# Performance work log

Hardware: AMD Instinct MI355X
Metric: run time of the kernel (lower is better)

The kernel has to match this reference:

```python
import jax, jax.numpy as jnp
import numpy as np

R = 5  # box filter radius (self.r)
EPS = 0.01


def box_filter(x, r):
    # depthwise (groups=C) box filter, kernel (2r+1)x(2r+1), zero padding r
    c = x.shape[1]
    k = 2 * r + 1
    w = jnp.full((c, 1, k, k), 1.0 / (k * k), dtype=x.dtype)
    return jax.lax.conv_general_dilated(
        x, w, window_strides=(1, 1), padding=[(r, r), (r, r)],
        dimension_numbers=("NCHW", "OIHW", "NCHW"), feature_group_count=c)


def setup_inputs() -> dict:
    key = jax.random.key(0)
    x = jax.random.normal(key, (4, 64, 256, 256), dtype=jnp.float32)
    return {"x": x}


def reference(x):
    _, _, H, W = x.shape
    # normalization map accounting for zero-padded borders
    N = box_filter(jnp.ones((1, 1, H, W), dtype=x.dtype), R)  # [1,1,H,W]
    mean_x = box_filter(x, R) / N
    var_x = box_filter(x * x, R) / N - mean_x * mean_x
    A = var_x / (var_x + EPS)
    b = (1.0 - A) * mean_x
    m = A * x + b
    return x * m
```

## Files before the change

### kernel.cpp

```cpp
#include <hip/hip_runtime.h>
#include <hip/hip_bf16.h>


#define RAD    5
#define KW     11
#define IMG_H  256
#define IMG_W  256
#define TILE_H 8
#define IN_H   (TILE_H + 2 * RAD)
#define STRIPS (IMG_H / TILE_H)
#define EPS_F  0.01f

__global__ __launch_bounds__(256)
void AdaGuidedFilter_17686675325295_kernel(const float* __restrict__ x,
                                           float* __restrict__ out) {
    __shared__ float2 vsum[TILE_H * IMG_W];

    const int d     = blockIdx.x;
    const int L     = (d & 7) * ((256 * STRIPS) / 8) + (d >> 3);
    const int img   = L >> 5;
    const int strip = L & (STRIPS - 1);
    const int tid   = threadIdx.x;

    const float* __restrict__ xim = x   + (size_t)img * (IMG_H * IMG_W);
    float* __restrict__       oim = out + (size_t)img * (IMG_H * IMG_W);

    const int row0 = strip * TILE_H - RAD;

    {
        float xr[IN_H];
        if (strip != 0 && strip != STRIPS - 1) {
            #pragma unroll
            for (int li = 0; li < IN_H; ++li)
                xr[li] = xim[(size_t)(row0 + li) * IMG_W + tid];
        } else {
            #pragma unroll
            for (int li = 0; li < IN_H; ++li) {
                const int g = row0 + li;
                xr[li] = (g >= 0 && g < IMG_H) ? xim[(size_t)g * IMG_W + tid] : 0.0f;
            }
        }

        float s = 0.0f, s2 = 0.0f;
        #pragma unroll
        for (int li = 0; li < KW; ++li) { s += xr[li]; s2 = fmaf(xr[li], xr[li], s2); }

        #pragma unroll
        for (int r = 0; r < TILE_H; ++r) {
            vsum[(r << 8) | (tid ^ r)] = make_float2(s, s2);
            if (r < TILE_H - 1) {
                const float a = xr[r + KW], b0 = xr[r];
                s  += a - b0;
                s2 += a * a - b0 * b0;
            }
        }
    }
    __syncthreads();

    const int lr  = tid & 7;
    const int seg = tid >> 3;
    const int c0  = seg * 8;
    const int gr  = strip * TILE_H + lr;

    float xv[8];
    {
        const float4* p = reinterpret_cast<const float4*>(xim + (size_t)gr * IMG_W + c0);
        const float4 q0 = p[0], q1 = p[1];
        xv[0]=q0.x; xv[1]=q0.y; xv[2]=q0.z; xv[3]=q0.w;
        xv[4]=q1.x; xv[5]=q1.y; xv[6]=q1.z; xv[7]=q1.w;
    }

    const int rlo = (gr - RAD < 0) ? 0 : gr - RAD;
    const int rhi = (gr + RAD > IMG_H - 1) ? IMG_H - 1 : gr + RAD;
    const float rcnt = (float)(rhi - rlo + 1);

    float o[8];
    if (seg >= 1 && seg <= 30) {
        float s = 0.0f, s2 = 0.0f;
        #pragma unroll
        for (int dd = -RAD; dd <= RAD; ++dd) {
            const float2 v = vsum[(lr << 8) | ((c0 + dd) ^ lr)];
            s += v.x; s2 += v.y;
        }
        const float inv = __builtin_amdgcn_rcpf(rcnt * 11.0f);
        #pragma unroll
        for (int i = 0; i < 8; ++i) {
            const float mean = s * inv;
            const float m2   = s2 * inv;
            const float var  = fmaf(-mean, mean, m2);
            const float A    = var * __builtin_amdgcn_rcpf(var + EPS_F);
            const float xq   = xv[i];
            o[i] = xq * fmaf(A, xq - mean, mean);
            if (i < 7) {
                const float2 va = vsum[(lr << 8) | ((c0 + i + RAD + 1) ^ lr)];
                const float2 vb = vsum[(lr << 8) | ((c0 + i - RAD) ^ lr)];
                s  += va.x - vb.x;
                s2 += va.y - vb.y;
            }
        }
    } else {
        float s = 0.0f, s2 = 0.0f;
        #pragma unroll
        for (int dd = -RAD; dd <= RAD; ++dd) {
            const int cc = c0 + dd;
            if (cc >= 0 && cc < IMG_W) {
                const float2 v = vsum[(lr << 8) | (cc ^ lr)];
                s += v.x; s2 += v.y;
            }
        }
        #pragma unroll
        for (int i = 0; i < 8; ++i) {
            const int c   = c0 + i;
            const int wlo = (c - RAD < 0) ? 0 : c - RAD;
            const int whi = (c + RAD > IMG_W - 1) ? IMG_W - 1 : c + RAD;
            const float inv  = __builtin_amdgcn_rcpf(rcnt * (float)(whi - wlo + 1));
            const float mean = s * inv;
            const float m2   = s2 * inv;
            const float var  = fmaf(-mean, mean, m2);
            const float A    = var * __builtin_amdgcn_rcpf(var + EPS_F);
            const float xq   = xv[i];
            o[i] = xq * fmaf(A, xq - mean, mean);
            if (i < 7) {
                const int ca = c + RAD + 1;
                const int cs = c - RAD;
                if (ca < IMG_W) { const float2 v = vsum[(lr << 8) | (ca ^ lr)]; s += v.x; s2 += v.y; }
                if (cs >= 0)    { const float2 v = vsum[(lr << 8) | (cs ^ lr)]; s -= v.x; s2 -= v.y; }
            }
        }
    }

    float4* orow = reinterpret_cast<float4*>(oim + (size_t)gr * IMG_W + c0);
    orow[0] = make_float4(o[0], o[1], o[2], o[3]);
    orow[1] = make_float4(o[4], o[5], o[6], o[7]);
}

extern "C" void kernel_launch(void* const* d_in, const int* in_sizes, int n_in,
                              void* d_out, int out_size, void* d_ws, size_t ws_size,
                              hipStream_t stream) {
    (void)in_sizes; (void)n_in; (void)d_ws; (void)ws_size; (void)out_size;
    const float* x = (const float*)d_in[0];
    float* out = (float*)d_out;
    dim3 grid(256 * STRIPS);
    dim3 block(256);
    AdaGuidedFilter_17686675325295_kernel<<<grid, block, 0, stream>>>(x, out);
}
```

Baseline: 29.13 us.

## Process taller strips per block with rolling vertical sums in chunks

Each block now covers a 32-row strip instead of 8 rows. It keeps a register ring buffer of 11 rows so the vertical running sum slides down the strip, and handles it in four 8-row chunks that reuse one shared-memory buffer. This cuts the redundant halo-row reads from 10 extra rows per 8 output rows to 10 per 32. In exchange the grid has four times fewer blocks, each chunk adds barriers, and the horizontal pass waits on the vertical pass inside each block.

```diff
diff --git a/kernel.cpp b/kernel.cpp
--- a/kernel.cpp
+++ b/kernel.cpp
@@ -6,70 +6,21 @@
 #define KW     11
 #define IMG_H  256
 #define IMG_W  256
-#define TILE_H 8
-#define IN_H   (TILE_H + 2 * RAD)
+#define TILE_H 32
+#define CHUNK  8
+#define NCHUNK (TILE_H / CHUNK)
 #define STRIPS (IMG_H / TILE_H)
+#define NBLK   (256 * STRIPS)
 #define EPS_F  0.01f
 
-__global__ __launch_bounds__(256)
-void AdaGuidedFilter_17686675325295_kernel(const float* __restrict__ x,
-                                           float* __restrict__ out) {
-    __shared__ float2 vsum[TILE_H * IMG_W];
+__device__ __forceinline__ float ldrow(const float* __restrict__ xim, int g, int c) {
+    return (g >= 0 && g < IMG_H) ? xim[(size_t)g * IMG_W + c] : 0.0f;
+}
 
-    const int d     = blockIdx.x;
-    const int L     = (d & 7) * ((256 * STRIPS) / 8) + (d >> 3);
-    const int img   = L >> 5;
-    const int strip = L & (STRIPS - 1);
-    const int tid   = threadIdx.x;
-
-    const float* __restrict__ xim = x   + (size_t)img * (IMG_H * IMG_W);
-    float* __restrict__       oim = out + (size_t)img * (IMG_H * IMG_W);
-
-    const int row0 = strip * TILE_H - RAD;
-
-    {
-        float xr[IN_H];
-        if (strip != 0 && strip != STRIPS - 1) {
-            #pragma unroll
-            for (int li = 0; li < IN_H; ++li)
-                xr[li] = xim[(size_t)(row0 + li) * IMG_W + tid];
-        } else {
-            #pragma unroll
-            for (int li = 0; li < IN_H; ++li) {
-                const int g = row0 + li;
-                xr[li] = (g >= 0 && g < IMG_H) ? xim[(size_t)g * IMG_W + tid] : 0.0f;
-            }
-        }
-
-        float s = 0.0f, s2 = 0.0f;
-        #pragma unroll
-        for (int li = 0; li < KW; ++li) { s += xr[li]; s2 = fmaf(xr[li], xr[li], s2); }
-
-        #pragma unroll
-        for (int r = 0; r < TILE_H; ++r) {
-            vsum[(r << 8) | (tid ^ r)] = make_float2(s, s2);
-            if (r < TILE_H - 1) {
-                const float a = xr[r + KW], b0 = xr[r];
-                s  += a - b0;
-                s2 += a * a - b0 * b0;
-            }
-        }
-    }
-    __syncthreads();
-
-    const int lr  = tid & 7;
-    const int seg = tid >> 3;
-    const int c0  = seg * 8;
-    const int gr  = strip * TILE_H + lr;
-
-    float xv[8];
-    {
-        const float4* p = reinterpret_cast<const float4*>(xim + (size_t)gr * IMG_W + c0);
-        const float4 q0 = p[0], q1 = p[1];
-        xv[0]=q0.x; xv[1]=q0.y; xv[2]=q0.z; xv[3]=q0.w;
-        xv[4]=q1.x; xv[5]=q1.y; xv[6]=q1.z; xv[7]=q1.w;
-    }
-
+__device__ __forceinline__ void half_pass(const float2* __restrict__ vsum,
+                                          float* __restrict__ oim,
+                                          const float* xv,
+                                          int lr, int seg, int c0, int gr) {
     const int rlo = (gr - RAD < 0) ? 0 : gr - RAD;
     const int rhi = (gr + RAD > IMG_H - 1) ? IMG_H - 1 : gr + RAD;
     const float rcnt = (float)(rhi - rlo + 1);
@@ -134,13 +85,84 @@
     orow[1] = make_float4(o[4], o[5], o[6], o[7]);
 }
 
+template<bool CHECKED>
+__device__ __forceinline__ void run_strip(const float* __restrict__ xim,
+                                          float* __restrict__ oim,
+                                          float2* __restrict__ vsum,
+                                          int strip, int tid) {
+    const int row0 = strip * TILE_H - RAD;
+    const int lr   = tid & 7;
+    const int seg  = tid >> 3;
+    const int c0   = seg * 8;
+
+    float ring[KW];
+    #pragma unroll
+    for (int i = 0; i < KW; ++i)
+        ring[i] = CHECKED ? ldrow(xim, row0 + i, tid)
+                          : xim[(size_t)(row0 + i) * IMG_W + tid];
+
+    float s = 0.0f, s2 = 0.0f;
+    #pragma unroll
+    for (int i = 0; i < KW; ++i) { s += ring[i]; s2 = fmaf(ring[i], ring[i], s2); }
+
+    #pragma unroll
+    for (int k = 0; k < NCHUNK; ++k) {
+        #pragma unroll
+        for (int rr = 0; rr < CHUNK; ++rr) {
+            const int r = k * CHUNK + rr;
+            vsum[(rr << 8) | (tid ^ rr)] = make_float2(s, s2);
+            if (r < TILE_H - 1) {
+                const float old = ring[r % KW];
+                const float a   = CHECKED ? ldrow(xim, row0 + KW + r, tid)
+                                          : xim[(size_t)(row0 + KW + r) * IMG_W + tid];
+                s  += a - old;
+                s2  = fmaf(a, a, fmaf(-old, old, s2));
+                ring[r % KW] = a;
+            }
+        }
+
+        const int gr = strip * TILE_H + k * CHUNK + lr;
+        float xv[8];
+        {
+            const float4* p = reinterpret_cast<const float4*>(xim + (size_t)gr * IMG_W + c0);
+            const float4 q0 = p[0], q1 = p[1];
+            xv[0]=q0.x; xv[1]=q0.y; xv[2]=q0.z; xv[3]=q0.w;
+            xv[4]=q1.x; xv[5]=q1.y; xv[6]=q1.z; xv[7]=q1.w;
+        }
+
+        __syncthreads();
+        half_pass(vsum, oim, xv, lr, seg, c0, gr);
+        if (k < NCHUNK - 1) __syncthreads();
+    }
+}
+
+__global__ __launch_bounds__(256)
+void AdaGuidedFilter_17686675325295_kernel(const float* __restrict__ x,
+                                           float* __restrict__ out) {
+    __shared__ float2 vsum[CHUNK * IMG_W];
+
+    const int d     = blockIdx.x;
+    const int L     = (d & 7) * (NBLK / 8) + (d >> 3);
+    const int img   = L >> 3;
+    const int strip = L & (STRIPS - 1);
+    const int tid   = threadIdx.x;
+
+    const float* __restrict__ xim = x   + (size_t)img * (IMG_H * IMG_W);
+    float* __restrict__       oim = out + (size_t)img * (IMG_H * IMG_W);
+
+    if (strip != 0 && strip != STRIPS - 1)
+        run_strip<false>(xim, oim, vsum, strip, tid);
+    else
+        run_strip<true>(xim, oim, vsum, strip, tid);
+}
+
 extern "C" void kernel_launch(void* const* d_in, const int* in_sizes, int n_in,
                               void* d_out, int out_size, void* d_ws, size_t ws_size,
                               hipStream_t stream) {
     (void)in_sizes; (void)n_in; (void)d_ws; (void)ws_size; (void)out_size;
     const float* x = (const float*)d_in[0];
     float* out = (float*)d_out;
-    dim3 grid(256 * STRIPS);
+    dim3 grid(NBLK);
     dim3 block(256);
     AdaGuidedFilter_17686675325295_kernel<<<grid, block, 0, stream>>>(x, out);
 }
```

Result: slower. 35.88 us (+23.2%).

## Split vertical pass across half the threads with float2 loads and packed math

Applied to the files above, without the earlier changes.

The vertical box-sum pass now runs on only the first 128 threads. Each handles two adjacent columns using 8-byte vector loads and packed f32x2 arithmetic, and writes float4 entries into the swizzled shared buffer. The other 128 threads issue their own row loads for the horizontal stage at the same time, so global loads from both stages overlap. The interior horizontal pass is restructured to compute two output columns per step with packed two-wide ops, aiming at v_pk_fma/v_pk_mul use. The cost is an imbalanced first phase where half the threads sit idle until the barrier.

```diff
diff --git a/kernel.cpp b/kernel.cpp
--- a/kernel.cpp
+++ b/kernel.cpp
@@ -9,7 +9,10 @@
 #define TILE_H 8
 #define IN_H   (TILE_H + 2 * RAD)
 #define STRIPS (IMG_H / TILE_H)
+#define NBLK   (256 * STRIPS)
 #define EPS_F  0.01f
+
+typedef float f32x2 __attribute__((ext_vector_type(2)));
 
 __global__ __launch_bounds__(256)
 void AdaGuidedFilter_17686675325295_kernel(const float* __restrict__ x,
@@ -17,58 +20,75 @@
     __shared__ float2 vsum[TILE_H * IMG_W];
 
     const int d     = blockIdx.x;
-    const int L     = (d & 7) * ((256 * STRIPS) / 8) + (d >> 3);
+    const int L     = (d & 7) * (NBLK / 8) + (d >> 3);
     const int img   = L >> 5;
     const int strip = L & (STRIPS - 1);
-    const int tid   = threadIdx.x;
+    const int t     = threadIdx.x;
 
     const float* __restrict__ xim = x   + (size_t)img * (IMG_H * IMG_W);
     float* __restrict__       oim = out + (size_t)img * (IMG_H * IMG_W);
 
     const int row0 = strip * TILE_H - RAD;
+    const bool rowcheck = (strip == 0) || (strip == STRIPS - 1);
 
-    {
-        float xr[IN_H];
-        if (strip != 0 && strip != STRIPS - 1) {
-            #pragma unroll
-            for (int li = 0; li < IN_H; ++li)
-                xr[li] = xim[(size_t)(row0 + li) * IMG_W + tid];
-        } else {
-            #pragma unroll
-            for (int li = 0; li < IN_H; ++li) {
-                const int g = row0 + li;
-                xr[li] = (g >= 0 && g < IMG_H) ? xim[(size_t)g * IMG_W + tid] : 0.0f;
-            }
-        }
-
-        float s = 0.0f, s2 = 0.0f;
-        #pragma unroll
-        for (int li = 0; li < KW; ++li) { s += xr[li]; s2 = fmaf(xr[li], xr[li], s2); }
-
-        #pragma unroll
-        for (int r = 0; r < TILE_H; ++r) {
-            vsum[(r << 8) | (tid ^ r)] = make_float2(s, s2);
-            if (r < TILE_H - 1) {
-                const float a = xr[r + KW], b0 = xr[r];
-                s  += a - b0;
-                s2 += a * a - b0 * b0;
-            }
-        }
-    }
-    __syncthreads();
-
-    const int lr  = tid & 7;
-    const int seg = tid >> 3;
+    const int lr  = t & 7;
+    const int seg = t >> 3;
     const int c0  = seg * 8;
     const int gr  = strip * TILE_H + lr;
 
     float xv[8];
-    {
+    if (t >= 128) {
         const float4* p = reinterpret_cast<const float4*>(xim + (size_t)gr * IMG_W + c0);
         const float4 q0 = p[0], q1 = p[1];
         xv[0]=q0.x; xv[1]=q0.y; xv[2]=q0.z; xv[3]=q0.w;
         xv[4]=q1.x; xv[5]=q1.y; xv[6]=q1.z; xv[7]=q1.w;
     }
+
+    if (t < 128) {
+        const int cc0 = t << 1;
+        f32x2 xr[IN_H];
+        if (!rowcheck) {
+            #pragma unroll
+            for (int li = 0; li < IN_H; ++li)
+                xr[li] = *reinterpret_cast<const f32x2*>(xim + (size_t)(row0 + li) * IMG_W + cc0);
+        } else {
+            #pragma unroll
+            for (int li = 0; li < IN_H; ++li) {
+                const int g = row0 + li;
+                if (g >= 0 && g < IMG_H)
+                    xr[li] = *reinterpret_cast<const f32x2*>(xim + (size_t)g * IMG_W + cc0);
+                else
+                    xr[li] = (f32x2){0.0f, 0.0f};
+            }
+        }
+
+        f32x2 s = {0.0f, 0.0f}, s2 = {0.0f, 0.0f};
+        #pragma unroll
+        for (int li = 0; li < KW; ++li) {
+            s += xr[li];
+            s2 = __builtin_elementwise_fma(xr[li], xr[li], s2);
+        }
+
+        float4* vs4 = reinterpret_cast<float4*>(vsum);
+        #pragma unroll
+        for (int r = 0; r < TILE_H; ++r) {
+            const int bi = (r << 7) | ((cc0 ^ r) >> 1);
+            if ((r & 1) == 0) vs4[bi] = make_float4(s.x, s2.x, s.y, s2.y);
+            else              vs4[bi] = make_float4(s.y, s2.y, s.x, s2.x);
+            if (r < TILE_H - 1) {
+                const f32x2 a = xr[r + KW], b = xr[r];
+                s  += a - b;
+                s2  = __builtin_elementwise_fma(a, a,
+                        __builtin_elementwise_fma(-b, b, s2));
+            }
+        }
+
+        const float4* p = reinterpret_cast<const float4*>(xim + (size_t)gr * IMG_W + c0);
+        const float4 q0 = p[0], q1 = p[1];
+        xv[0]=q0.x; xv[1]=q0.y; xv[2]=q0.z; xv[3]=q0.w;
+        xv[4]=q1.x; xv[5]=q1.y; xv[6]=q1.z; xv[7]=q1.w;
+    }
+    __syncthreads();
 
     const int rlo = (gr - RAD < 0) ? 0 : gr - RAD;
     const int rhi = (gr + RAD > IMG_H - 1) ? IMG_H - 1 : gr + RAD;
@@ -83,19 +103,35 @@
             s += v.x; s2 += v.y;
         }
         const float inv = __builtin_amdgcn_rcpf(rcnt * 11.0f);
+        const f32x2 inv2  = {inv, inv};
+        const f32x2 eps2  = {EPS_F, EPS_F};
+
         #pragma unroll
-        for (int i = 0; i < 8; ++i) {
-            const float mean = s * inv;
-            const float m2   = s2 * inv;
-            const float var  = fmaf(-mean, mean, m2);
-            const float A    = var * __builtin_amdgcn_rcpf(var + EPS_F);
-            const float xq   = xv[i];
-            o[i] = xq * fmaf(A, xq - mean, mean);
-            if (i < 7) {
-                const float2 va = vsum[(lr << 8) | ((c0 + i + RAD + 1) ^ lr)];
-                const float2 vb = vsum[(lr << 8) | ((c0 + i - RAD) ^ lr)];
-                s  += va.x - vb.x;
-                s2 += va.y - vb.y;
+        for (int g = 0; g < 4; ++g) {
+            const int ce = c0 + 2 * g;
+            const float2 va = vsum[(lr << 8) | ((ce + RAD + 1) ^ lr)];
+            const float2 vb = vsum[(lr << 8) | ((ce - RAD) ^ lr)];
+            const float so  = s  + va.x - vb.x;
+            const float s2o = s2 + va.y - vb.y;
+            const f32x2 SS   = {s, so};
+            const f32x2 SS2  = {s2, s2o};
+            const f32x2 mean = SS * inv2;
+            const f32x2 m2   = SS2 * inv2;
+            const f32x2 var  = __builtin_elementwise_fma(-mean, mean, m2);
+            const f32x2 den  = var + eps2;
+            const f32x2 rr   = {__builtin_amdgcn_rcpf(den.x), __builtin_amdgcn_rcpf(den.y)};
+            const f32x2 A    = var * rr;
+            const f32x2 xq   = {xv[2*g], xv[2*g+1]};
+            const f32x2 xm   = xq - mean;
+            const f32x2 tt   = __builtin_elementwise_fma(A, xm, mean);
+            const f32x2 oo   = xq * tt;
+            o[2*g]   = oo.x;
+            o[2*g+1] = oo.y;
+            if (g < 3) {
+                const float2 va2 = vsum[(lr << 8) | ((ce + RAD + 2) ^ lr)];
+                const float2 vb2 = vsum[(lr << 8) | ((ce - RAD + 1) ^ lr)];
+                s  = so  + va2.x - vb2.x;
+                s2 = s2o + va2.y - vb2.y;
             }
         }
     } else {
@@ -140,7 +176,7 @@
     (void)in_sizes; (void)n_in; (void)d_ws; (void)ws_size; (void)out_size;
     const float* x = (const float*)d_in[0];
     float* out = (float*)d_out;
-    dim3 grid(256 * STRIPS);
+    dim3 grid(NBLK);
     dim3 block(256);
     AdaGuidedFilter_17686675325295_kernel<<<grid, block, 0, stream>>>(x, out);
 }
```

After: 31.34 us. +7.6%, slower.

## Split tile into per-wavefront column slabs with halo to drop block barrier

Applied to the files above, without the earlier changes.

Each 64-lane wavefront now owns a 64-column slab and computes its own vertical sums, including a 10-column halo, into a private LDS region. The block-wide __syncthreads is replaced by an lgkmcnt wait, which relies on wavefront-synchronous execution. The aim is to remove block-level barrier stalls so wavefronts run independently. In exchange, halo columns are reloaded and summed redundantly (about 16% extra column work), and 10 lanes do a second column pass, which causes divergence.

```diff
diff --git a/kernel.cpp b/kernel.cpp
--- a/kernel.cpp
+++ b/kernel.cpp
@@ -9,79 +9,85 @@
 #define TILE_H 8
 #define IN_H   (TILE_H + 2 * RAD)
 #define STRIPS (IMG_H / TILE_H)
+#define NBLK   (256 * STRIPS)
+#define WSTR   80
 #define EPS_F  0.01f
 
-__global__ __launch_bounds__(256)
-void AdaGuidedFilter_17686675325295_kernel(const float* __restrict__ x,
-                                           float* __restrict__ out) {
-    __shared__ float2 vsum[TILE_H * IMG_W];
+__device__ __forceinline__ int swz(int co, int r) {
+    return (co & ~7) | ((co & 7) ^ r);
+}
 
-    const int d     = blockIdx.x;
-    const int L     = (d & 7) * ((256 * STRIPS) / 8) + (d >> 3);
-    const int img   = L >> 5;
-    const int strip = L & (STRIPS - 1);
-    const int tid   = threadIdx.x;
+template<bool ROWCHECK>
+__device__ __forceinline__ void colpass(const float* __restrict__ xim,
+                                        float2* __restrict__ vb,
+                                        int row0, int gc, bool colok, int co) {
+    float xr[IN_H];
+    #pragma unroll
+    for (int li = 0; li < IN_H; ++li) {
+        const int g = row0 + li;
+        const bool ok = colok && (!ROWCHECK || ((unsigned)g < (unsigned)IMG_H));
+        xr[li] = ok ? xim[(size_t)g * IMG_W + gc] : 0.0f;
+    }
+    float s = 0.0f, s2 = 0.0f;
+    #pragma unroll
+    for (int li = 0; li < KW; ++li) { s += xr[li]; s2 = fmaf(xr[li], xr[li], s2); }
+    #pragma unroll
+    for (int r = 0; r < TILE_H; ++r) {
+        vb[r * WSTR + swz(co, r)] = make_float2(s, s2);
+        if (r < TILE_H - 1) {
+            const float a = xr[r + KW], b = xr[r];
+            s  += a - b;
+            s2  = fmaf(a, a, fmaf(-b, b, s2));
+        }
+    }
+}
 
-    const float* __restrict__ xim = x   + (size_t)img * (IMG_H * IMG_W);
-    float* __restrict__       oim = out + (size_t)img * (IMG_H * IMG_W);
-
+template<bool ROWCHECK>
+__device__ __forceinline__ void run_tile(const float* __restrict__ xim,
+                                         float* __restrict__ oim,
+                                         float2* __restrict__ vb,
+                                         int strip, int C0, int l) {
     const int row0 = strip * TILE_H - RAD;
 
+    if (l < 10) {
+        const int gc = C0 + 59 + l;
+        colpass<ROWCHECK>(xim, vb, row0, gc, gc < IMG_W, 64 + l);
+    }
     {
-        float xr[IN_H];
-        if (strip != 0 && strip != STRIPS - 1) {
-            #pragma unroll
-            for (int li = 0; li < IN_H; ++li)
-                xr[li] = xim[(size_t)(row0 + li) * IMG_W + tid];
-        } else {
-            #pragma unroll
-            for (int li = 0; li < IN_H; ++li) {
-                const int g = row0 + li;
-                xr[li] = (g >= 0 && g < IMG_H) ? xim[(size_t)g * IMG_W + tid] : 0.0f;
-            }
-        }
+        const int gc = C0 - 5 + l;
+        colpass<ROWCHECK>(xim, vb, row0, gc, (unsigned)gc < (unsigned)IMG_W, l);
+    }
 
-        float s = 0.0f, s2 = 0.0f;
-        #pragma unroll
-        for (int li = 0; li < KW; ++li) { s += xr[li]; s2 = fmaf(xr[li], xr[li], s2); }
-
-        #pragma unroll
-        for (int r = 0; r < TILE_H; ++r) {
-            vsum[(r << 8) | (tid ^ r)] = make_float2(s, s2);
-            if (r < TILE_H - 1) {
-                const float a = xr[r + KW], b0 = xr[r];
-                s  += a - b0;
-                s2 += a * a - b0 * b0;
-            }
-        }
-    }
-    __syncthreads();
-
-    const int lr  = tid & 7;
-    const int seg = tid >> 3;
-    const int c0  = seg * 8;
-    const int gr  = strip * TILE_H + lr;
+    const int lr    = l & 7;
+    const int seg   = l >> 3;
+    const int gcol0 = C0 + seg * 8;
+    const int gr    = strip * TILE_H + lr;
 
     float xv[8];
     {
-        const float4* p = reinterpret_cast<const float4*>(xim + (size_t)gr * IMG_W + c0);
+        const float4* p = reinterpret_cast<const float4*>(xim + (size_t)gr * IMG_W + gcol0);
         const float4 q0 = p[0], q1 = p[1];
         xv[0]=q0.x; xv[1]=q0.y; xv[2]=q0.z; xv[3]=q0.w;
         xv[4]=q1.x; xv[5]=q1.y; xv[6]=q1.z; xv[7]=q1.w;
     }
 
+    asm volatile("s_waitcnt lgkmcnt(0)" ::: "memory");
+
     const int rlo = (gr - RAD < 0) ? 0 : gr - RAD;
     const int rhi = (gr + RAD > IMG_H - 1) ? IMG_H - 1 : gr + RAD;
     const float rcnt = (float)(rhi - rlo + 1);
 
+    const int cob = seg * 8;
+    float s = 0.0f, s2 = 0.0f;
+    #pragma unroll
+    for (int dd = 0; dd < KW; ++dd) {
+        const float2 v = vb[lr * WSTR + swz(cob + dd, lr)];
+        s += v.x; s2 += v.y;
+    }
+
     float o[8];
-    if (seg >= 1 && seg <= 30) {
-        float s = 0.0f, s2 = 0.0f;
-        #pragma unroll
-        for (int dd = -RAD; dd <= RAD; ++dd) {
-            const float2 v = vsum[(lr << 8) | ((c0 + dd) ^ lr)];
-            s += v.x; s2 += v.y;
-        }
+    const bool edge = (C0 == 0 && seg == 0) || (C0 == 192 && seg == 7);
+    if (!edge) {
         const float inv = __builtin_amdgcn_rcpf(rcnt * 11.0f);
         #pragma unroll
         for (int i = 0; i < 8; ++i) {
@@ -92,25 +98,16 @@
             const float xq   = xv[i];
             o[i] = xq * fmaf(A, xq - mean, mean);
             if (i < 7) {
-                const float2 va = vsum[(lr << 8) | ((c0 + i + RAD + 1) ^ lr)];
-                const float2 vb = vsum[(lr << 8) | ((c0 + i - RAD) ^ lr)];
-                s  += va.x - vb.x;
-                s2 += va.y - vb.y;
+                const float2 va = vb[lr * WSTR + swz(cob + i + KW, lr)];
+                const float2 vs = vb[lr * WSTR + swz(cob + i, lr)];
+                s  += va.x - vs.x;
+                s2 += va.y - vs.y;
             }
         }
     } else {
-        float s = 0.0f, s2 = 0.0f;
-        #pragma unroll
-        for (int dd = -RAD; dd <= RAD; ++dd) {
-            const int cc = c0 + dd;
-            if (cc >= 0 && cc < IMG_W) {
-                const float2 v = vsum[(lr << 8) | (cc ^ lr)];
-                s += v.x; s2 += v.y;
-            }
-        }
         #pragma unroll
         for (int i = 0; i < 8; ++i) {
-            const int c   = c0 + i;
+            const int c   = gcol0 + i;
             const int wlo = (c - RAD < 0) ? 0 : c - RAD;
             const int whi = (c + RAD > IMG_W - 1) ? IMG_W - 1 : c + RAD;
             const float inv  = __builtin_amdgcn_rcpf(rcnt * (float)(whi - wlo + 1));
@@ -121,17 +118,41 @@
             const float xq   = xv[i];
             o[i] = xq * fmaf(A, xq - mean, mean);
             if (i < 7) {
-                const int ca = c + RAD + 1;
-                const int cs = c - RAD;
-                if (ca < IMG_W) { const float2 v = vsum[(lr << 8) | (ca ^ lr)]; s += v.x; s2 += v.y; }
-                if (cs >= 0)    { const float2 v = vsum[(lr << 8) | (cs ^ lr)]; s -= v.x; s2 -= v.y; }
+                const float2 va = vb[lr * WSTR + swz(cob + i + KW, lr)];
+                const float2 vs = vb[lr * WSTR + swz(cob + i, lr)];
+                s  += va.x - vs.x;
+                s2 += va.y - vs.y;
             }
         }
     }
 
-    float4* orow = reinterpret_cast<float4*>(oim + (size_t)gr * IMG_W + c0);
+    float4* orow = reinterpret_cast<float4*>(oim + (size_t)gr * IMG_W + gcol0);
     orow[0] = make_float4(o[0], o[1], o[2], o[3]);
     orow[1] = make_float4(o[4], o[5], o[6], o[7]);
+}
+
+__global__ __launch_bounds__(256)
+void AdaGuidedFilter_17686675325295_kernel(const float* __restrict__ x,
+                                           float* __restrict__ out) {
+    __shared__ float2 lds[4 * TILE_H * WSTR];
+
+    const int d     = blockIdx.x;
+    const int L     = (d & 7) * (NBLK / 8) + (d >> 3);
+    const int img   = L >> 5;
+    const int strip = L & (STRIPS - 1);
+    const int t     = threadIdx.x;
+    const int wid   = t >> 6;
+    const int l     = t & 63;
+    const int C0    = wid << 6;
+
+    const float* __restrict__ xim = x   + (size_t)img * (IMG_H * IMG_W);
+    float* __restrict__       oim = out + (size_t)img * (IMG_H * IMG_W);
+    float2* __restrict__      vb  = lds + wid * (TILE_H * WSTR);
+
+    if (strip != 0 && strip != STRIPS - 1)
+        run_tile<false>(xim, oim, vb, strip, C0, l);
+    else
+        run_tile<true>(xim, oim, vb, strip, C0, l);
 }
 
 extern "C" void kernel_launch(void* const* d_in, const int* in_sizes, int n_in,
@@ -140,7 +161,7 @@
     (void)in_sizes; (void)n_in; (void)d_ws; (void)ws_size; (void)out_size;
     const float* x = (const float*)d_in[0];
     float* out = (float*)d_out;
-    dim3 grid(256 * STRIPS);
+    dim3 grid(NBLK);
     dim3 block(256);
     AdaGuidedFilter_17686675325295_kernel<<<grid, block, 0, stream>>>(x, out);
 }
```

Result: slower. 34.72 us (+19.2%).
